# Kernel tuning notes

Hardware: AMD Instinct MI355X
Metric: run time of the kernel (lower is better)

Reference implementation:

```python
import jax, jax.numpy as jnp
import numpy as np

N_NODES = 100000
N_EDGES = 1600000
IN_DIM = 128
HEADS = 4
HEAD_DIM = 16  # hidden_dim 64 // 4 heads
HID = HEADS * HEAD_DIM
NEG_SLOPE = 0.2


def setup_inputs() -> dict:
    key = jax.random.key(0)
    ks = jax.random.split(key, 20)
    inp = {
        "x": jax.random.normal(ks[0], (N_NODES, IN_DIM), dtype=jnp.float32),
        "edge_index": jax.random.randint(ks[1], (2, N_EDGES), 0, N_NODES, dtype=jnp.int32),
    }
    dims = [IN_DIM, HID, HID]
    for l in range(3):
        d_in = dims[l]
        sc = 1.0 / np.sqrt(d_in)
        inp[f"w{l}"] = jax.random.normal(ks[2 + 4 * l], (d_in, HID), dtype=jnp.float32) * sc
        inp[f"asrc{l}"] = jax.random.normal(ks[3 + 4 * l], (HEADS, HEAD_DIM), dtype=jnp.float32) * 0.1
        inp[f"adst{l}"] = jax.random.normal(ks[4 + 4 * l], (HEADS, HEAD_DIM), dtype=jnp.float32) * 0.1
        inp[f"b{l}"] = jnp.zeros((HID,), dtype=jnp.float32)
    inp["out_w"] = jax.random.normal(ks[14], (HID, 1), dtype=jnp.float32) * (1.0 / np.sqrt(HID))
    inp["out_b"] = jnp.zeros((1,), dtype=jnp.float32)
    return inp


def _gat_layer(h, src, dst, W, a_src, a_dst, b):
    # h: [N, d_in]; src/dst: [E'] (self-loops already appended)
    n = h.shape[0]
    xh = (h @ W).reshape(n, HEADS, HEAD_DIM)              # [N,H,C]
    al_s = jnp.sum(xh * a_src, axis=-1)                   # [N,H]
    al_d = jnp.sum(xh * a_dst, axis=-1)                   # [N,H]
    e = jax.nn.leaky_relu(al_s[src] + al_d[dst], NEG_SLOPE)  # [E',H]
    # segment-softmax over incoming edges of each destination node
    m = jax.ops.segment_max(e, dst, num_segments=n)       # [N,H]
    p = jnp.exp(e - m[dst])
    z = jax.ops.segment_sum(p, dst, num_segments=n)       # [N,H]
    alpha = p / (z[dst] + 1e-16)                          # [E',H]
    msg = xh[src] * alpha[:, :, None]                     # [E',H,C]
    out = jax.ops.segment_sum(msg, dst, num_segments=n)   # [N,H,C]
    return out.reshape(n, HID) + b


def reference(x, edge_index, w0, asrc0, adst0, b0, w1, asrc1, adst1, b1,
              w2, asrc2, adst2, b2, out_w, out_b):
    n = x.shape[0]
    loops = jnp.arange(n, dtype=edge_index.dtype)
    src = jnp.concatenate([edge_index[0], loops])  # PyG GATConv adds self-loops
    dst = jnp.concatenate([edge_index[1], loops])
    h = x
    params = [(w0, asrc0, adst0, b0), (w1, asrc1, adst1, b1), (w2, asrc2, adst2, b2)]
    for W, a_s, a_d, b in params:
        h = _gat_layer(h, src, dst, W, a_s, a_d, b)
        h = jax.nn.relu(h)
    return (h @ out_w + out_b).squeeze(-1)  # [N]
```

## Files before the change

kernel.cpp:

```cpp
#include <hip/hip_runtime.h>


#define NBMAX 512
#define SCHUNK 4096
#define BCAP 8192
#define PADSLACK 768

typedef __attribute__((ext_vector_type(8))) short bf16x8;
typedef __attribute__((ext_vector_type(4))) float f32x4;

__device__ inline unsigned short bf16_rtn(float x) {
    union { float f; unsigned u; } a; a.f = x;
    return (unsigned short)((a.u + 0x7FFFu + ((a.u >> 16) & 1u)) >> 16);
}
__device__ inline float bf16_to_f(unsigned short s) {
    union { unsigned u; float f; } b; b.u = ((unsigned)s) << 16;
    return b.f;
}

__global__ __launch_bounds__(256) void k_prep(const float* __restrict__ w0, const float* __restrict__ w1,
                                              const float* __restrict__ w2,
                                              unsigned short* __restrict__ p0h, unsigned short* __restrict__ p0l,
                                              unsigned short* __restrict__ p1h, unsigned short* __restrict__ p1l,
                                              unsigned short* __restrict__ p2h, unsigned short* __restrict__ p2l,
                                              int* __restrict__ bhist, float* __restrict__ als,
                                              float* __restrict__ xh, int n) {
    int bid = blockIdx.x, t = threadIdx.x;
    if (bid == 8) {
        bhist[t] = 0;
        bhist[t + 256] = 0;
        if (t < 4) als[(size_t)n * 4 + t] = -1e30f;
        if (t < 64) xh[(size_t)n * 64 + t] = 0.f;
        return;
    }
    int g = bid * 256 + t;
    const float* W;
    unsigned short *ph, *pl;
    int idx;
    if (g < 1024) { W = w0; ph = p0h; pl = p0l; idx = g; }
    else if (g < 1536) { W = w1; ph = p1h; pl = p1l; idx = g - 1024; }
    else if (g < 2048) { W = w2; ph = p2h; pl = p2l; idx = g - 1536; }
    else return;
    int ko = idx >> 6, nn = idx & 63;
#pragma unroll
    for (int j = 0; j < 8; ++j) {
        float w = W[(size_t)(ko * 8 + j) * 64 + nn];
        unsigned short hb = bf16_rtn(w);
        ph[(size_t)idx * 8 + j] = hb;
        pl[(size_t)idx * 8 + j] = bf16_rtn(w - bf16_to_f(hb));
    }
}

__global__ __launch_bounds__(256) void k_bhist(const int* __restrict__ dst, int* __restrict__ bhist, int e) {
    __shared__ unsigned int h[NBMAX];
    int t = threadIdx.x;
    h[t] = 0;
    h[t + 256] = 0;
    __syncthreads();
    for (int i = blockIdx.x * 256 + t; i < e; i += gridDim.x * 256)
        atomicAdd(&h[dst[i] >> 8], 1u);
    __syncthreads();
    if (h[t]) atomicAdd(&bhist[t], (int)h[t]);
    if (h[t + 256]) atomicAdd(&bhist[t + 256], (int)h[t + 256]);
}

__global__ __launch_bounds__(512) void k_bscan(const int* __restrict__ bhist, int* __restrict__ boffs,
                                               int* __restrict__ bfill, int nb, int e) {
    __shared__ int s[NBMAX];
    int t = threadIdx.x;
    int v = (t < nb) ? bhist[t] : 0;
    s[t] = v;
    __syncthreads();
    for (int o = 1; o < 512; o <<= 1) {
        int add = (t >= o) ? s[t - o] : 0;
        __syncthreads();
        s[t] += add;
        __syncthreads();
    }
    boffs[t] = s[t] - v;
    if (t == 511) boffs[512] = s[511];
    bfill[t] = 0;
}

template <int D_IN>
__device__ __forceinline__ void mgemm_wave(const float* __restrict__ h,
                                           const unsigned short* __restrict__ wph,
                                           const unsigned short* __restrict__ wpl,
                                           const float* __restrict__ asrc, const float* __restrict__ adst,
                                           float* __restrict__ xh, float* __restrict__ als,
                                           float* __restrict__ ald, float* __restrict__ mvec,
                                           int m0, int lane, int n) {
    int quad = lane >> 4, l16 = lane & 15;
    int node_a = m0 + l16;
    int mm = min(node_a, n - 1);
    const float* hrow = h + (size_t)mm * D_IN + quad * 8;

    f32x4 acc[4];
#pragma unroll
    for (int i = 0; i < 4; ++i) acc[i] = (f32x4){0.f, 0.f, 0.f, 0.f};

    constexpr int KSTEPS = D_IN / 32;
#pragma unroll
    for (int s = 0; s < KSTEPS; ++s) {
        float4 a0 = *(const float4*)(hrow + s * 32);
        float4 a1 = *(const float4*)(hrow + s * 32 + 4);
        float av[8] = {a0.x, a0.y, a0.z, a0.w, a1.x, a1.y, a1.z, a1.w};
        bf16x8 ahi, alo;
#pragma unroll
        for (int j = 0; j < 8; ++j) {
            unsigned short hb = bf16_rtn(av[j]);
            ahi[j] = (short)hb;
            alo[j] = (short)bf16_rtn(av[j] - bf16_to_f(hb));
        }
        const unsigned short* bbase = wph + ((size_t)((s * 4 + quad) * 64 + l16)) * 8;
        const unsigned short* bbasel = wpl + ((size_t)((s * 4 + quad) * 64 + l16)) * 8;
#pragma unroll
        for (int nt = 0; nt < 4; ++nt) {
            bf16x8 bhi = *(const bf16x8*)(bbase + (size_t)nt * 16 * 8);
            bf16x8 blo = *(const bf16x8*)(bbasel + (size_t)nt * 16 * 8);
            acc[nt] = __builtin_amdgcn_mfma_f32_16x16x32_bf16(ahi, bhi, acc[nt], 0, 0, 0);
            acc[nt] = __builtin_amdgcn_mfma_f32_16x16x32_bf16(ahi, blo, acc[nt], 0, 0, 0);
            acc[nt] = __builtin_amdgcn_mfma_f32_16x16x32_bf16(alo, bhi, acc[nt], 0, 0, 0);
        }
    }
#pragma unroll
    for (int nt = 0; nt < 4; ++nt) {
        float as_l = asrc[nt * 16 + l16];
        float ad_l = adst[nt * 16 + l16];
#pragma unroll
        for (int r = 0; r < 4; ++r) {
            int node = m0 + quad * 4 + r;
            float c = acc[nt][r];
            if (node < n) xh[(size_t)node * 64 + nt * 16 + l16] = c;
            float ps = c * as_l, pd = c * ad_l;
            ps += __shfl_xor(ps, 1, 64); pd += __shfl_xor(pd, 1, 64);
            ps += __shfl_xor(ps, 2, 64); pd += __shfl_xor(pd, 2, 64);
            ps += __shfl_xor(ps, 4, 64); pd += __shfl_xor(pd, 4, 64);
            ps += __shfl_xor(ps, 8, 64); pd += __shfl_xor(pd, 8, 64);
            if (l16 == 0 && node < n) {
                als[node * 4 + nt] = ps;
                ald[node * 4 + nt] = pd;
                float sm = ps + pd;
                mvec[node * 4 + nt] = sm >= 0.f ? sm : 0.2f * sm;
            }
        }
    }
}

template <int D_IN>
__global__ __launch_bounds__(256) void k_mgemm(const float* __restrict__ h,
                                               const unsigned short* __restrict__ wph,
                                               const unsigned short* __restrict__ wpl,
                                               const float* __restrict__ asrc, const float* __restrict__ adst,
                                               float* __restrict__ xh, float* __restrict__ als,
                                               float* __restrict__ ald, float* __restrict__ mvec, int n) {
    int t = threadIdx.x;
    int m0 = blockIdx.x * 64 + (t >> 6) * 16;
    mgemm_wave<D_IN>(h, wph, wpl, asrc, adst, xh, als, ald, mvec, m0, t & 63, n);
}

__global__ __launch_bounds__(512) void k_mix1(const int* __restrict__ src, const int* __restrict__ dst,
                                              const int* __restrict__ boffs, int* __restrict__ bfill,
                                              unsigned int* __restrict__ edata, int e, int sb,
                                              const float* __restrict__ x,
                                              const unsigned short* __restrict__ p0h,
                                              const unsigned short* __restrict__ p0l,
                                              const float* __restrict__ asrc, const float* __restrict__ adst,
                                              float* __restrict__ xh, float* __restrict__ als,
                                              float* __restrict__ ald, float* __restrict__ mvec, int n) {
    __shared__ unsigned int hist[NBMAX];
    __shared__ unsigned int loc[NBMAX];
    __shared__ int gbase[NBMAX];
    __shared__ unsigned int stmp[NBMAX];
    __shared__ unsigned int sortbuf[SCHUNK];
    __shared__ int posbuf[SCHUNK];
    int t = threadIdx.x;
    if (blockIdx.x >= sb) {
        int mblk = blockIdx.x - sb;
        int m0 = mblk * 128 + (t >> 6) * 16;
        mgemm_wave<128>(x, p0h, p0l, asrc, adst, xh, als, ald, mvec, m0, t & 63, n);
        return;
    }
    int i0 = blockIdx.x * SCHUNK;
    int cnt = min(SCHUNK, e - i0);
    hist[t] = 0;
    __syncthreads();
    for (int j = t; j < cnt; j += 512) atomicAdd(&hist[dst[i0 + j] >> 8], 1u);
    __syncthreads();
    unsigned int v = hist[t];
    stmp[t] = v;
    __syncthreads();
    for (int o = 1; o < 512; o <<= 1) {
        unsigned int add = (t >= o) ? stmp[t - o] : 0;
        __syncthreads();
        stmp[t] += add;
        __syncthreads();
    }
    loc[t] = stmp[t] - v;
    int gb = 0;
    if (v > 0) gb = atomicAdd(&bfill[t], (int)v);
    gbase[t] = boffs[t] + gb - (int)loc[t];
    hist[t] = loc[t];
    __syncthreads();
    for (int j = t; j < cnt; j += 512) {
        int d = dst[i0 + j];
        int s = src[i0 + j];
        int b = d >> 8;
        unsigned int p = atomicAdd(&hist[b], 1u);
        sortbuf[p] = (unsigned int)s | ((unsigned int)(d & 255) << 24);
        posbuf[p] = gbase[b] + (int)p;
    }
    __syncthreads();
    for (int j = t; j < cnt; j += 512) edata[posbuf[j]] = sortbuf[j];
}

__global__ __launch_bounds__(512) void k_mix2(const unsigned int* __restrict__ edata,
                                              const int* __restrict__ boffs, int* __restrict__ poffs,
                                              int* __restrict__ pend, int* __restrict__ ssrc,
                                              int n, int nb, int mg1,
                                              const float* __restrict__ x,
                                              const unsigned short* __restrict__ p0h,
                                              const unsigned short* __restrict__ p0l,
                                              const float* __restrict__ asrc, const float* __restrict__ adst,
                                              float* __restrict__ xh, float* __restrict__ als,
                                              float* __restrict__ ald, float* __restrict__ mvec) {
    __shared__ unsigned int hist[256];
    __shared__ unsigned int stmp[256];
    __shared__ unsigned int loc2[256];
    __shared__ unsigned int srcbuf[BCAP];
    int t = threadIdx.x;
    if (blockIdx.x >= nb) {
        int mblk = mg1 + (blockIdx.x - nb);
        int m0 = mblk * 128 + (t >> 6) * 16;
        mgemm_wave<128>(x, p0h, p0l, asrc, adst, xh, als, ald, mvec, m0, t & 63, n);
        return;
    }
    int b = blockIdx.x;
    int e0 = boffs[b], e1 = boffs[b + 1];
    int cnt = e1 - e0;
    int pb = e0 + b * PADSLACK;
    if (t < 256) hist[t] = 0;
    __syncthreads();
    for (int j = t; j < cnt; j += 512) atomicAdd(&hist[edata[e0 + j] >> 24], 1u);
    __syncthreads();
    unsigned int v = 0, v4 = 0;
    if (t < 256) {
        v = hist[t];
        v4 = (v + 3u) & ~3u;
        stmp[t] = v4;
    }
    __syncthreads();
    for (int o = 1; o < 256; o <<= 1) {
        unsigned int add = 0;
        if (t < 256 && t >= o) add = stmp[t - o];
        __syncthreads();
        if (t < 256) stmp[t] += add;
        __syncthreads();
    }
    int ptot = (int)stmp[255];
    if (t < 256) {
        loc2[t] = stmp[t] - v4;
        int node = b * 256 + t;
        if (node < n) {
            poffs[node] = pb + (int)loc2[t];
            pend[node] = pb + (int)(loc2[t] + v4);
        }
        hist[t] = loc2[t];
    }
    __syncthreads();
    if (cnt + PADSLACK <= BCAP) {
        for (int j = t; j < cnt; j += 512) {
            unsigned int p = edata[e0 + j];
            unsigned int pos = atomicAdd(&hist[p >> 24], 1u);
            srcbuf[pos] = p & 0xFFFFFFu;
        }
        if (t < 256)
            for (unsigned int k = v; k < v4; ++k) srcbuf[loc2[t] + k] = (unsigned int)n;
        __syncthreads();
        for (int j = t; j < ptot; j += 512) ssrc[pb + j] = (int)srcbuf[j];
    } else {
        for (int j = t; j < cnt; j += 512) {
            unsigned int p = edata[e0 + j];
            unsigned int pos = atomicAdd(&hist[p >> 24], 1u);
            ssrc[pb + (int)pos] = (int)(p & 0xFFFFFFu);
        }
        if (t < 256)
            for (unsigned int k = v; k < v4; ++k) ssrc[pb + (int)(loc2[t] + k)] = n;
    }
}

__device__ inline float4 lrelu4(float4 v) {
    float4 r;
    r.x = v.x >= 0.f ? v.x : 0.2f * v.x;
    r.y = v.y >= 0.f ? v.y : 0.2f * v.y;
    r.z = v.z >= 0.f ? v.z : 0.2f * v.z;
    r.w = v.w >= 0.f ? v.w : 0.2f * v.w;
    return r;
}

#define ACCUM(LO, HI, ACCA, ACCB, ZS)                                           \
    {                                                                           \
        int g_ = ((LO) - s0) >> 2, gb_ = ((HI) - s0) >> 2;                      \
        for (; g_ + 4 <= gb_; g_ += 4) {                                        \
            int4 uu0 = *(const int4*)&ub[g_ * 4];                               \
            int4 uu1 = *(const int4*)&ub[g_ * 4 + 4];                           \
            int4 uu2 = *(const int4*)&ub[g_ * 4 + 8];                           \
            int4 uu3 = *(const int4*)&ub[g_ * 4 + 12];                          \
            float4 pp0 = *(const float4*)&per[g_ * 4];                          \
            float4 pp1 = *(const float4*)&per[g_ * 4 + 4];                      \
            float4 pp2 = *(const float4*)&per[g_ * 4 + 8];                      \
            float4 pp3 = *(const float4*)&per[g_ * 4 + 12];                     \
            float x0 = *(const float*)(xl + (size_t)(unsigned)uu0.x);           \
            float x1 = *(const float*)(xl + (size_t)(unsigned)uu0.y);           \
            float x2 = *(const float*)(xl + (size_t)(unsigned)uu0.z);           \
            float x3 = *(const float*)(xl + (size_t)(unsigned)uu0.w);           \
            float x4 = *(const float*)(xl + (size_t)(unsigned)uu1.x);           \
            float x5 = *(const float*)(xl + (size_t)(unsigned)uu1.y);           \
            float x6 = *(const float*)(xl + (size_t)(unsigned)uu1.z);           \
            float x7 = *(const float*)(xl + (size_t)(unsigned)uu1.w);           \
            float x8 = *(const float*)(xl + (size_t)(unsigned)uu2.x);           \
            float x9 = *(const float*)(xl + (size_t)(unsigned)uu2.y);           \
            float xa = *(const float*)(xl + (size_t)(unsigned)uu2.z);           \
            float xb = *(const float*)(xl + (size_t)(unsigned)uu2.w);           \
            float xc = *(const float*)(xl + (size_t)(unsigned)uu3.x);           \
            float xd = *(const float*)(xl + (size_t)(unsigned)uu3.y);           \
            float xe = *(const float*)(xl + (size_t)(unsigned)uu3.z);           \
            float xf = *(const float*)(xl + (size_t)(unsigned)uu3.w);           \
            ZS += pp0.x + pp0.y + pp0.z + pp0.w;                                \
            ZS += pp1.x + pp1.y + pp1.z + pp1.w;                                \
            ZS += pp2.x + pp2.y + pp2.z + pp2.w;                                \
            ZS += pp3.x + pp3.y + pp3.z + pp3.w;                                \
            ACCA += pp0.x * x0; ACCB += pp0.y * x1;                             \
            ACCA += pp0.z * x2; ACCB += pp0.w * x3;                             \
            ACCA += pp1.x * x4; ACCB += pp1.y * x5;                             \
            ACCA += pp1.z * x6; ACCB += pp1.w * x7;                             \
            ACCA += pp2.x * x8; ACCB += pp2.y * x9;                             \
            ACCA += pp2.z * xa; ACCB += pp2.w * xb;                             \
            ACCA += pp3.x * xc; ACCB += pp3.y * xd;                             \
            ACCA += pp3.z * xe; ACCB += pp3.w * xf;                             \
        }                                                                       \
        for (; g_ < gb_; ++g_) {                                                \
            int4 uu = *(const int4*)&ub[g_ * 4];                                \
            float4 pp = *(const float4*)&per[g_ * 4];                           \
            float x0 = *(const float*)(xl + (size_t)(unsigned)uu.x);            \
            float x1 = *(const float*)(xl + (size_t)(unsigned)uu.y);            \
            float x2 = *(const float*)(xl + (size_t)(unsigned)uu.z);            \
            float x3 = *(const float*)(xl + (size_t)(unsigned)uu.w);            \
            ZS += pp.x + pp.y + pp.z + pp.w;                                    \
            ACCA += pp.x * x0; ACCB += pp.y * x1;                               \
            ACCA += pp.z * x2; ACCB += pp.w * x3;                               \
        }                                                                       \
    }

__global__ __launch_bounds__(256) void k_agg(const float* __restrict__ xh,
                                             const float* __restrict__ als, const float* __restrict__ ald,
                                             const float* __restrict__ mvec,
                                             const int* __restrict__ poffs, const int* __restrict__ pend,
                                             const int* __restrict__ ssrc,
                                             const float* __restrict__ bias, float* __restrict__ hout,
                                             const float* __restrict__ outw, const float* __restrict__ outb,
                                             float* __restrict__ fout, int n) {
    __shared__ int s_u[4][64];
    __shared__ float s_pe[4][4][64];
    int wslot = threadIdx.x >> 6;
    int lane = threadIdx.x & 63;
    int w = (blockIdx.x * 256 + threadIdx.x) >> 6;
    int v0 = w << 2;
    if (v0 >= n) return;
    int head = lane >> 4;
    int* ub = s_u[wslot];
    float* per = s_pe[wslot][head];
    float* pew = &s_pe[wslot][0][lane];

    int vlast = n - 1;
    int last = min(v0 + 3, vlast);
    int4 rr = *(const int4*)(poffs + v0);
    int e3 = pend[last];
    int r0 = rr.x;
    int r1 = (v0 + 1 <= last) ? rr.y : e3;
    int r2 = (v0 + 2 <= last) ? rr.z : e3;
    int r3 = (v0 + 3 <= last) ? rr.w : e3;

    const char* xl = (const char*)(xh + lane);
    float acc0a = *(const float*)(xl + ((size_t)(unsigned)v0 << 8));
    float acc1a = *(const float*)(xl + ((size_t)(unsigned)min(v0 + 1, vlast) << 8));
    float acc2a = *(const float*)(xl + ((size_t)(unsigned)min(v0 + 2, vlast) << 8));
    float acc3a = *(const float*)(xl + ((size_t)(unsigned)min(v0 + 3, vlast) << 8));
    float acc0b = 0.f, acc1b = 0.f, acc2b = 0.f, acc3b = 0.f;
    float zs0 = 0.f, zs1 = 0.f, zs2 = 0.f, zs3 = 0.f;

    int s0 = r0;
    int u_n = n;
    if (s0 < e3) {
        if (lane < e3 - s0) u_n = ssrc[s0 + lane];
    }
    float4 alu_n = *(const float4*)(als + 4 * (size_t)u_n);
    int e_n = s0 + lane;
    int nid_n = min(v0 + (e_n >= r1) + (e_n >= r2) + (e_n >= r3), vlast);
    float4 ald_n = *(const float4*)(ald + 4 * (size_t)nid_n);
    float4 m_n = *(const float4*)(mvec + 4 * (size_t)nid_n);

    while (s0 < e3) {
        int cnt = min(64, e3 - s0);
        float4 e4 = lrelu4(make_float4(alu_n.x + ald_n.x, alu_n.y + ald_n.y,
                                       alu_n.z + ald_n.z, alu_n.w + ald_n.w));
        float4 pe;
        pe.x = __expf(e4.x - m_n.x);
        pe.y = __expf(e4.y - m_n.y);
        pe.z = __expf(e4.z - m_n.z);
        pe.w = __expf(e4.w - m_n.w);
        ub[lane] = u_n << 8;
        pew[0] = pe.x;
        pew[64] = pe.y;
        pew[128] = pe.z;
        pew[192] = pe.w;
        int s1 = s0 + 64;
        if (s1 < e3) {
            u_n = n;
            if (lane < e3 - s1) u_n = ssrc[s1 + lane];
            alu_n = *(const float4*)(als + 4 * (size_t)u_n);
            int e1 = s1 + lane;
            int nid1 = min(v0 + (e1 >= r1) + (e1 >= r2) + (e1 >= r3), vlast);
            ald_n = *(const float4*)(ald + 4 * (size_t)nid1);
            m_n = *(const float4*)(mvec + 4 * (size_t)nid1);
        }
        int lim = s0 + cnt;
        int hi0 = min(r1, lim);
        int lo1 = max(r1, s0), hi1 = min(r2, lim);
        int lo2 = max(r2, s0), hi2 = min(r3, lim);
        int lo3 = max(r3, s0);
        ACCUM(s0, hi0, acc0a, acc0b, zs0);
        ACCUM(lo1, hi1, acc1a, acc1b, zs1);
        ACCUM(lo2, hi2, acc2a, acc2b, zs2);
        ACCUM(lo3, lim, acc3a, acc3b, zs3);
        s0 = s1;
    }

    float bl = bias[lane];
    float o0 = fmaxf((acc0a + acc0b) / (1.f + zs0 + 1e-16f) + bl, 0.f);
    float o1 = fmaxf((acc1a + acc1b) / (1.f + zs1 + 1e-16f) + bl, 0.f);
    float o2 = fmaxf((acc2a + acc2b) / (1.f + zs2 + 1e-16f) + bl, 0.f);
    float o3 = fmaxf((acc3a + acc3b) / (1.f + zs3 + 1e-16f) + bl, 0.f);
    if (outw) {
        float ow = outw[lane];
        float ob = outb[0];
        float t0 = o0 * ow, t1 = o1 * ow, t2 = o2 * ow, t3 = o3 * ow;
#pragma unroll
        for (int d = 32; d; d >>= 1) {
            t0 += __shfl_down(t0, d, 64);
            t1 += __shfl_down(t1, d, 64);
            t2 += __shfl_down(t2, d, 64);
            t3 += __shfl_down(t3, d, 64);
        }
        if (lane == 0) {
            fout[v0] = t0 + ob;
            if (v0 + 1 < n) fout[v0 + 1] = t1 + ob;
            if (v0 + 2 < n) fout[v0 + 2] = t2 + ob;
            if (v0 + 3 < n) fout[v0 + 3] = t3 + ob;
        }
    } else {
        hout[((size_t)v0 << 6) + lane] = o0;
        if (v0 + 1 < n) hout[((size_t)(v0 + 1) << 6) + lane] = o1;
        if (v0 + 2 < n) hout[((size_t)(v0 + 2) << 6) + lane] = o2;
        if (v0 + 3 < n) hout[((size_t)(v0 + 3) << 6) + lane] = o3;
    }
}

extern "C" void kernel_launch(void* const* d_in, const int* in_sizes, int n_in,
                              void* d_out, int out_size, void* d_ws, size_t ws_size,
                              hipStream_t stream) {
    const float* x = (const float*)d_in[0];
    const int* ei = (const int*)d_in[1];
    const float* w[3] = {(const float*)d_in[2], (const float*)d_in[6], (const float*)d_in[10]};
    const float* as[3] = {(const float*)d_in[3], (const float*)d_in[7], (const float*)d_in[11]};
    const float* ad[3] = {(const float*)d_in[4], (const float*)d_in[8], (const float*)d_in[12]};
    const float* b[3] = {(const float*)d_in[5], (const float*)d_in[9], (const float*)d_in[13]};
    const float* outw = (const float*)d_in[14];
    const float* outb = (const float*)d_in[15];

    const int N = in_sizes[0] / 128;
    const int E = in_sizes[1] / 2;
    const int* src = ei;
    const int* dst = ei + E;
    const int NB = (N + 255) / 256;
    const int SB = (E + SCHUNK - 1) / SCHUNK;
    const int GB128 = (N + 127) / 128;
    const int MG1 = (GB128 + 1) / 2;
    const int MG2 = GB128 - MG1;

    char* ws = (char*)d_ws;
    auto alloc = [&](size_t bytes) -> void* {
        void* p = (void*)ws;
        ws += (bytes + 255) & ~(size_t)255;
        return p;
    };
    int* bhist = (int*)alloc(NBMAX * 4);
    int* boffs = (int*)alloc((NBMAX + 1) * 4);
    int* bfill = (int*)alloc(NBMAX * 4);
    int* poffs = (int*)alloc((size_t)(N + 8) * 4);
    int* pend = (int*)alloc((size_t)N * 4);
    int* ssrc = (int*)alloc((size_t)(E + NBMAX * PADSLACK + 256) * 4);
    unsigned int* edata = (unsigned int*)alloc((size_t)(E + 64) * 4);
    float* xh = (float*)alloc((size_t)(N + 1) * 64 * 4);
    float* hbuf = (float*)alloc((size_t)N * 64 * 4);
    float* als = (float*)alloc((size_t)(N + 1) * 4 * 4);
    float* ald = (float*)alloc((size_t)N * 4 * 4);
    float* mvec = (float*)alloc((size_t)N * 4 * 4);
    unsigned short* p0h = (unsigned short*)alloc(8192 * 2);
    unsigned short* p0l = (unsigned short*)alloc(8192 * 2);
    unsigned short* p1h = (unsigned short*)alloc(4096 * 2);
    unsigned short* p1l = (unsigned short*)alloc(4096 * 2);
    unsigned short* p2h = (unsigned short*)alloc(4096 * 2);
    unsigned short* p2l = (unsigned short*)alloc(4096 * 2);

    k_prep<<<9, 256, 0, stream>>>(w[0], w[1], w[2], p0h, p0l, p1h, p1l, p2h, p2l, bhist, als, xh, N);
    k_bhist<<<256, 256, 0, stream>>>(dst, bhist, E);
    k_bscan<<<1, 512, 0, stream>>>(bhist, boffs, bfill, NB, E);
    k_mix1<<<SB + MG1, 512, 0, stream>>>(src, dst, boffs, bfill, edata, E, SB,
                                         x, p0h, p0l, as[0], ad[0], xh, als, ald, mvec, N);
    k_mix2<<<NB + MG2, 512, 0, stream>>>(edata, boffs, poffs, pend, ssrc, N, NB, MG1,
                                         x, p0h, p0l, as[0], ad[0], xh, als, ald, mvec);

    const int gblocks = (N + 63) / 64;
    const int ablocks = (N + 15) / 16;

    k_agg<<<ablocks, 256, 0, stream>>>(xh, als, ald, mvec, poffs, pend, ssrc, b[0], hbuf, nullptr, nullptr, nullptr, N);
    k_mgemm<64><<<gblocks, 256, 0, stream>>>(hbuf, p1h, p1l, as[1], ad[1], xh, als, ald, mvec, N);
    k_agg<<<ablocks, 256, 0, stream>>>(xh, als, ald, mvec, poffs, pend, ssrc, b[1], hbuf, nullptr, nullptr, nullptr, N);
    k_mgemm<64><<<gblocks, 256, 0, stream>>>(hbuf, p2h, p2l, as[2], ad[2], xh, als, ald, mvec, N);
    k_agg<<<ablocks, 256, 0, stream>>>(xh, als, ald, mvec, poffs, pend, ssrc, b[2], nullptr, outw, outb, (float*)d_out, N);
}
```

Measured before the change: 426.6 us.

## Fuse next-layer linear projection and attention logits into aggregation kernel

Layers 1 and 2 no longer have a separate MFMA GEMM kernel. Each aggregation wave stages its four output rows in shared memory and multiplies them by a transposed fp32 weight matrix. It then computes the next layer's xh, alpha_src, alpha_dst and max seeds directly, using ping-pong buffers. This removes the hbuf write/read round trip and two kernel launches. In exchange the small matmul runs on scalar FP32 ALUs inside the latency-bound gather kernel, and the edge-data scratch now aliases the second xh buffer.

```diff
diff --git a/kernel.cpp b/kernel.cpp
--- a/kernel.cpp
+++ b/kernel.cpp
@@ -21,33 +21,42 @@
 __global__ __launch_bounds__(256) void k_prep(const float* __restrict__ w0, const float* __restrict__ w1,
                                               const float* __restrict__ w2,
                                               unsigned short* __restrict__ p0h, unsigned short* __restrict__ p0l,
-                                              unsigned short* __restrict__ p1h, unsigned short* __restrict__ p1l,
-                                              unsigned short* __restrict__ p2h, unsigned short* __restrict__ p2l,
-                                              int* __restrict__ bhist, float* __restrict__ als,
-                                              float* __restrict__ xh, int n) {
+                                              float* __restrict__ wt1, float* __restrict__ wt2,
+                                              int* __restrict__ bhist,
+                                              float* __restrict__ alsA, float* __restrict__ alsB,
+                                              float* __restrict__ xhA, float* __restrict__ xhB, int n) {
     int bid = blockIdx.x, t = threadIdx.x;
-    if (bid == 8) {
+    if (bid == 4) {
         bhist[t] = 0;
         bhist[t + 256] = 0;
-        if (t < 4) als[(size_t)n * 4 + t] = -1e30f;
-        if (t < 64) xh[(size_t)n * 64 + t] = 0.f;
+        if (t < 4) {
+            alsA[(size_t)n * 4 + t] = -1e30f;
+            alsB[(size_t)n * 4 + t] = -1e30f;
+        }
+        if (t < 64) {
+            xhA[(size_t)n * 64 + t] = 0.f;
+            xhB[(size_t)n * 64 + t] = 0.f;
+        }
         return;
     }
-    int g = bid * 256 + t;
-    const float* W;
-    unsigned short *ph, *pl;
-    int idx;
-    if (g < 1024) { W = w0; ph = p0h; pl = p0l; idx = g; }
-    else if (g < 1536) { W = w1; ph = p1h; pl = p1l; idx = g - 1024; }
-    else if (g < 2048) { W = w2; ph = p2h; pl = p2l; idx = g - 1536; }
-    else return;
+    if (bid >= 5) {
+        const float* W = (bid == 5) ? w1 : w2;
+        float* wt = (bid == 5) ? wt1 : wt2;
+#pragma unroll
+        for (int j = 0; j < 16; ++j) {
+            int e = t * 16 + j;
+            wt[e] = W[(size_t)(e & 63) * 64 + (e >> 6)];
+        }
+        return;
+    }
+    int idx = bid * 256 + t;
     int ko = idx >> 6, nn = idx & 63;
 #pragma unroll
     for (int j = 0; j < 8; ++j) {
-        float w = W[(size_t)(ko * 8 + j) * 64 + nn];
+        float w = w0[(size_t)(ko * 8 + j) * 64 + nn];
         unsigned short hb = bf16_rtn(w);
-        ph[(size_t)idx * 8 + j] = hb;
-        pl[(size_t)idx * 8 + j] = bf16_rtn(w - bf16_to_f(hb));
+        p0h[(size_t)idx * 8 + j] = hb;
+        p0l[(size_t)idx * 8 + j] = bf16_rtn(w - bf16_to_f(hb));
     }
 }
 
@@ -82,26 +91,24 @@
     bfill[t] = 0;
 }
 
-template <int D_IN>
-__device__ __forceinline__ void mgemm_wave(const float* __restrict__ h,
-                                           const unsigned short* __restrict__ wph,
-                                           const unsigned short* __restrict__ wpl,
-                                           const float* __restrict__ asrc, const float* __restrict__ adst,
-                                           float* __restrict__ xh, float* __restrict__ als,
-                                           float* __restrict__ ald, float* __restrict__ mvec,
-                                           int m0, int lane, int n) {
+__device__ __forceinline__ void mgemm_wave128(const float* __restrict__ h,
+                                              const unsigned short* __restrict__ wph,
+                                              const unsigned short* __restrict__ wpl,
+                                              const float* __restrict__ asrc, const float* __restrict__ adst,
+                                              float* __restrict__ xh, float* __restrict__ als,
+                                              float* __restrict__ ald, float* __restrict__ mvec,
+                                              int m0, int lane, int n) {
     int quad = lane >> 4, l16 = lane & 15;
     int node_a = m0 + l16;
     int mm = min(node_a, n - 1);
-    const float* hrow = h + (size_t)mm * D_IN + quad * 8;
+    const float* hrow = h + (size_t)mm * 128 + quad * 8;
 
     f32x4 acc[4];
 #pragma unroll
     for (int i = 0; i < 4; ++i) acc[i] = (f32x4){0.f, 0.f, 0.f, 0.f};
 
-    constexpr int KSTEPS = D_IN / 32;
-#pragma unroll
-    for (int s = 0; s < KSTEPS; ++s) {
+#pragma unroll
+    for (int s = 0; s < 4; ++s) {
         float4 a0 = *(const float4*)(hrow + s * 32);
         float4 a1 = *(const float4*)(hrow + s * 32 + 4);
         float av[8] = {a0.x, a0.y, a0.z, a0.w, a1.x, a1.y, a1.z, a1.w};
@@ -145,18 +152,6 @@
             }
         }
     }
-}
-
-template <int D_IN>
-__global__ __launch_bounds__(256) void k_mgemm(const float* __restrict__ h,
-                                               const unsigned short* __restrict__ wph,
-                                               const unsigned short* __restrict__ wpl,
-                                               const float* __restrict__ asrc, const float* __restrict__ adst,
-                                               float* __restrict__ xh, float* __restrict__ als,
-                                               float* __restrict__ ald, float* __restrict__ mvec, int n) {
-    int t = threadIdx.x;
-    int m0 = blockIdx.x * 64 + (t >> 6) * 16;
-    mgemm_wave<D_IN>(h, wph, wpl, asrc, adst, xh, als, ald, mvec, m0, t & 63, n);
 }
 
 __global__ __launch_bounds__(512) void k_mix1(const int* __restrict__ src, const int* __restrict__ dst,
@@ -178,7 +173,7 @@
     if (blockIdx.x >= sb) {
         int mblk = blockIdx.x - sb;
         int m0 = mblk * 128 + (t >> 6) * 16;
-        mgemm_wave<128>(x, p0h, p0l, asrc, adst, xh, als, ald, mvec, m0, t & 63, n);
+        mgemm_wave128(x, p0h, p0l, asrc, adst, xh, als, ald, mvec, m0, t & 63, n);
         return;
     }
     int i0 = blockIdx.x * SCHUNK;
@@ -232,7 +227,7 @@
     if (blockIdx.x >= nb) {
         int mblk = mg1 + (blockIdx.x - nb);
         int m0 = mblk * 128 + (t >> 6) * 16;
-        mgemm_wave<128>(x, p0h, p0l, asrc, adst, xh, als, ald, mvec, m0, t & 63, n);
+        mgemm_wave128(x, p0h, p0l, asrc, adst, xh, als, ald, mvec, m0, t & 63, n);
         return;
     }
     int b = blockIdx.x;
@@ -357,11 +352,16 @@
                                              const float* __restrict__ mvec,
                                              const int* __restrict__ poffs, const int* __restrict__ pend,
                                              const int* __restrict__ ssrc,
-                                             const float* __restrict__ bias, float* __restrict__ hout,
+                                             const float* __restrict__ bias,
+                                             const float* __restrict__ wtn, const float* __restrict__ asn,
+                                             const float* __restrict__ adn,
+                                             float* __restrict__ xho, float* __restrict__ also_,
+                                             float* __restrict__ aldo, float* __restrict__ mveco,
                                              const float* __restrict__ outw, const float* __restrict__ outb,
                                              float* __restrict__ fout, int n) {
     __shared__ int s_u[4][64];
     __shared__ float s_pe[4][4][64];
+    __shared__ float s_o[4][4][64];
     int wslot = threadIdx.x >> 6;
     int lane = threadIdx.x & 63;
     int w = (blockIdx.x * 256 + threadIdx.x) >> 6;
@@ -441,6 +441,7 @@
     float o1 = fmaxf((acc1a + acc1b) / (1.f + zs1 + 1e-16f) + bl, 0.f);
     float o2 = fmaxf((acc2a + acc2b) / (1.f + zs2 + 1e-16f) + bl, 0.f);
     float o3 = fmaxf((acc3a + acc3b) / (1.f + zs3 + 1e-16f) + bl, 0.f);
+
     if (outw) {
         float ow = outw[lane];
         float ob = outb[0];
@@ -458,11 +459,47 @@
             if (v0 + 2 < n) fout[v0 + 2] = t2 + ob;
             if (v0 + 3 < n) fout[v0 + 3] = t3 + ob;
         }
-    } else {
-        hout[((size_t)v0 << 6) + lane] = o0;
-        if (v0 + 1 < n) hout[((size_t)(v0 + 1) << 6) + lane] = o1;
-        if (v0 + 2 < n) hout[((size_t)(v0 + 2) << 6) + lane] = o2;
-        if (v0 + 3 < n) hout[((size_t)(v0 + 3) << 6) + lane] = o3;
+        return;
+    }
+
+    float* ob = &s_o[wslot][0][0];
+    ob[lane] = o0;
+    ob[64 + lane] = o1;
+    ob[128 + lane] = o2;
+    ob[192 + lane] = o3;
+    const float* wrow = wtn + (size_t)lane * 64;
+    float y0 = 0.f, y1 = 0.f, y2 = 0.f, y3 = 0.f;
+#pragma unroll 4
+    for (int k = 0; k < 64; k += 4) {
+        float4 wv = *(const float4*)(wrow + k);
+        float4 q0 = *(const float4*)(ob + k);
+        float4 q1 = *(const float4*)(ob + 64 + k);
+        float4 q2 = *(const float4*)(ob + 128 + k);
+        float4 q3 = *(const float4*)(ob + 192 + k);
+        y0 += q0.x * wv.x + q0.y * wv.y + q0.z * wv.z + q0.w * wv.w;
+        y1 += q1.x * wv.x + q1.y * wv.y + q1.z * wv.z + q1.w * wv.w;
+        y2 += q2.x * wv.x + q2.y * wv.y + q2.z * wv.z + q2.w * wv.w;
+        y3 += q3.x * wv.x + q3.y * wv.y + q3.z * wv.z + q3.w * wv.w;
+    }
+    float as_l = asn[lane], ad_l = adn[lane];
+#pragma unroll
+    for (int nd = 0; nd < 4; ++nd) {
+        int node = v0 + nd;
+        if (node >= n) break;
+        float y = nd == 0 ? y0 : nd == 1 ? y1 : nd == 2 ? y2 : y3;
+        xho[(size_t)node * 64 + lane] = y;
+        float ps = y * as_l, pd = y * ad_l;
+        ps += __shfl_xor(ps, 1, 64); pd += __shfl_xor(pd, 1, 64);
+        ps += __shfl_xor(ps, 2, 64); pd += __shfl_xor(pd, 2, 64);
+        ps += __shfl_xor(ps, 4, 64); pd += __shfl_xor(pd, 4, 64);
+        ps += __shfl_xor(ps, 8, 64); pd += __shfl_xor(pd, 8, 64);
+        if ((lane & 15) == 0) {
+            int h = lane >> 4;
+            also_[node * 4 + h] = ps;
+            aldo[node * 4 + h] = pd;
+            float sm = ps + pd;
+            mveco[node * 4 + h] = sm >= 0.f ? sm : 0.2f * sm;
+        }
     }
 }
 
@@ -500,33 +537,37 @@
     int* poffs = (int*)alloc((size_t)(N + 8) * 4);
     int* pend = (int*)alloc((size_t)N * 4);
     int* ssrc = (int*)alloc((size_t)(E + NBMAX * PADSLACK + 256) * 4);
-    unsigned int* edata = (unsigned int*)alloc((size_t)(E + 64) * 4);
-    float* xh = (float*)alloc((size_t)(N + 1) * 64 * 4);
-    float* hbuf = (float*)alloc((size_t)N * 64 * 4);
-    float* als = (float*)alloc((size_t)(N + 1) * 4 * 4);
-    float* ald = (float*)alloc((size_t)N * 4 * 4);
-    float* mvec = (float*)alloc((size_t)N * 4 * 4);
+    float* xhA = (float*)alloc((size_t)(N + 1) * 64 * 4);
+    float* xhB = (float*)alloc((size_t)(N + 1) * 64 * 4);
+    float* alsA = (float*)alloc((size_t)(N + 1) * 4 * 4);
+    float* alsB = (float*)alloc((size_t)(N + 1) * 4 * 4);
+    float* aldA = (float*)alloc((size_t)N * 4 * 4);
+    float* aldB = (float*)alloc((size_t)N * 4 * 4);
+    float* mvecA = (float*)alloc((size_t)N * 4 * 4);
+    float* mvecB = (float*)alloc((size_t)N * 4 * 4);
     unsigned short* p0h = (unsigned short*)alloc(8192 * 2);
     unsigned short* p0l = (unsigned short*)alloc(8192 * 2);
-    unsigned short* p1h = (unsigned short*)alloc(4096 * 2);
-    unsigned short* p1l = (unsigned short*)alloc(4096 * 2);
-    unsigned short* p2h = (unsigned short*)alloc(4096 * 2);
-    unsigned short* p2l = (unsigned short*)alloc(4096 * 2);
-
-    k_prep<<<9, 256, 0, stream>>>(w[0], w[1], w[2], p0h, p0l, p1h, p1l, p2h, p2l, bhist, als, xh, N);
+    float* wt1 = (float*)alloc(4096 * 4);
+    float* wt2 = (float*)alloc(4096 * 4);
+    unsigned int* edata = (unsigned int*)xhB;
+
+    k_prep<<<7, 256, 0, stream>>>(w[0], w[1], w[2], p0h, p0l, wt1, wt2, bhist, alsA, alsB, xhA, xhB, N);
     k_bhist<<<256, 256, 0, stream>>>(dst, bhist, E);
     k_bscan<<<1, 512, 0, stream>>>(bhist, boffs, bfill, NB, E);
     k_mix1<<<SB + MG1, 512, 0, stream>>>(src, dst, boffs, bfill, edata, E, SB,
-                                         x, p0h, p0l, as[0], ad[0], xh, als, ald, mvec, N);
+                                         x, p0h, p0l, as[0], ad[0], xhA, alsA, aldA, mvecA, N);
     k_mix2<<<NB + MG2, 512, 0, stream>>>(edata, boffs, poffs, pend, ssrc, N, NB, MG1,
-                                         x, p0h, p0l, as[0], ad[0], xh, als, ald, mvec);
-
-    const int gblocks = (N + 63) / 64;
+                                         x, p0h, p0l, as[0], ad[0], xhA, alsA, aldA, mvecA);
+
     const int ablocks = (N + 15) / 16;
 
-    k_agg<<<ablocks, 256, 0, stream>>>(xh, als, ald, mvec, poffs, pend, ssrc, b[0], hbuf, nullptr, nullptr, nullptr, N);
-    k_mgemm<64><<<gblocks, 256, 0, stream>>>(hbuf, p1h, p1l, as[1], ad[1], xh, als, ald, mvec, N);
-    k_agg<<<ablocks, 256, 0, stream>>>(xh, als, ald, mvec, poffs, pend, ssrc, b[1], hbuf, nullptr, nullptr, nullptr, N);
-    k_mgemm<64><<<gblocks, 256, 0, stream>>>(hbuf, p2h, p2l, as[2], ad[2], xh, als, ald, mvec, N);
-    k_agg<<<ablocks, 256, 0, stream>>>(xh, als, ald, mvec, poffs, pend, ssrc, b[2], nullptr, outw, outb, (float*)d_out, N);
-}
+    k_agg<<<ablocks, 256, 0, stream>>>(xhA, alsA, aldA, mvecA, poffs, pend, ssrc, b[0],
+                                       wt1, as[1], ad[1], xhB, alsB, aldB, mvecB,
+                                       nullptr, nullptr, nullptr, N);
+    k_agg<<<ablocks, 256, 0, stream>>>(xhB, alsB, aldB, mvecB, poffs, pend, ssrc, b[1],
+                                       wt2, as[2], ad[2], xhA, alsA, aldA, mvecA,
+                                       nullptr, nullptr, nullptr, N);
+    k_agg<<<ablocks, 256, 0, stream>>>(xhA, alsA, aldA, mvecA, poffs, pend, ssrc, b[2],
+                                       nullptr, nullptr, nullptr, nullptr, nullptr, nullptr, nullptr,
+                                       outw, outb, (float*)d_out, N);
+}
```

After: 463.4 us. 8.6% more time.
